# Kernel optimization log

Hardware: AMD Instinct MI355X
Metric: run time of the kernel (lower is better)

Reference implementation:

```python
import jax, jax.numpy as jnp
import numpy as np

N = 100000      # nodes
E = 1600000     # edges (avg degree 16)
IN = 128
HID = 128
OUT = 128
G = 512         # graphs in batch


def setup_inputs() -> dict:
    key = jax.random.key(0)
    ks = jax.random.split(key, 8)
    x = jax.random.normal(ks[0], (N, IN), dtype=jnp.float32)
    edge_index = jax.random.randint(ks[1], (2, E), 0, N, dtype=jnp.int64)
    batch = jnp.sort(jax.random.randint(ks[2], (N,), 0, G, dtype=jnp.int64))
    # GCNConv params: weight (glorot-ish) + zero bias, per layer
    W1 = jax.random.normal(ks[3], (IN, HID), dtype=jnp.float32) / np.sqrt(IN)
    b1 = jnp.zeros((HID,), jnp.float32)
    W2 = jax.random.normal(ks[4], (HID, OUT), dtype=jnp.float32) / np.sqrt(HID)
    b2 = jnp.zeros((OUT,), jnp.float32)
    return {"x": x, "edge_index": edge_index, "batch": batch,
            "W1": W1, "b1": b1, "W2": W2, "b2": b2}


def _gcn_layer(h, W, b, src, dst, norm, n):
    # linear transform then normalized scatter-add aggregation
    h = h @ W                                  # [N, F_out]
    msg = h[src] * norm[:, None]               # [E+N, F_out]
    out = jax.ops.segment_sum(msg, dst, num_segments=n)
    return out + b


def reference(x, edge_index, batch, W1, b1, W2, b2):
    x = x.astype(jnp.float32)
    n = x.shape[0]
    # GCNConv adds self-loops and uses symmetric deg^-1/2 normalization
    loop = jnp.arange(n)
    src = jnp.concatenate([edge_index[0], loop])
    dst = jnp.concatenate([edge_index[1], loop])
    deg = jax.ops.segment_sum(jnp.ones_like(dst, dtype=x.dtype), dst, num_segments=n)
    dis = jnp.where(deg > 0, jax.lax.rsqrt(jnp.maximum(deg, 1.0)), 0.0)
    norm = dis[src] * dis[dst]                 # [E+N]

    h = jax.nn.relu(_gcn_layer(x, W1, b1, src, dst, norm, n))
    # dropout p=0.0 -> identity
    h = jax.nn.relu(_gcn_layer(h, W2, b2, src, dst, norm, n))

    # global_mean_pool over batch ids
    sums = jax.ops.segment_sum(h, batch, num_segments=G)          # [G, OUT]
    counts = jax.ops.segment_sum(jnp.ones((n,), h.dtype), batch, num_segments=G)
    return sums / jnp.maximum(counts, 1.0)[:, None]
```

## Files before the change

### kernel.cpp

```cpp
#include <hip/hip_runtime.h>
#include <stddef.h>


#define F 128
#define EB 4096
#define BSH 9

typedef unsigned int uint;
typedef unsigned short ushort;
typedef __attribute__((ext_vector_type(8))) short s16x8;
typedef __attribute__((ext_vector_type(4))) float f32x4;

__device__ __forceinline__ float bf_lo(uint v) { return __uint_as_float(v << 16); }
__device__ __forceinline__ float bf_hi(uint v) { return __uint_as_float(v & 0xffff0000u); }
__device__ __forceinline__ ushort f2bf(float f) {
    uint u = __float_as_uint(f);
    u += 0x7fffu + ((u >> 16) & 1u);
    return (ushort)(u >> 16);
}
__device__ __forceinline__ uint pack_bf2(float lo, float hi) {
    return (uint)f2bf(lo) | ((uint)f2bf(hi) << 16);
}

__device__ __forceinline__ int scan256_incl(int* s, int t, int v) {
    s[t] = v;
    __syncthreads();
#pragma unroll
    for (int d = 1; d < 256; d <<= 1) {
        int y = (t >= d) ? s[t - d] : 0;
        __syncthreads();
        s[t] += y;
        __syncthreads();
    }
    return s[t];
}


__global__ __launch_bounds__(256) void passA_kernel(const int* __restrict__ ei,
                                                    int* __restrict__ bucket_cnt,
                                                    int e, int nbuc) {
    __shared__ int h[256];
    int t = threadIdx.x;
    h[t] = 0;
    __syncthreads();
    for (int i = blockIdx.x * 256 + t; i < e; i += gridDim.x * 256)
        atomicAdd(&h[ei[e + i] >> BSH], 1);
    __syncthreads();
    if (t < nbuc && h[t]) atomicAdd(&bucket_cnt[t], h[t]);
}


__global__ __launch_bounds__(256) void scanb_kernel(const int* __restrict__ bucket_cnt,
                                                    int* __restrict__ bucket_base,
                                                    int* __restrict__ gcur, int nbuc) {
    __shared__ int aux[256];
    int t = threadIdx.x;
    int v = (t < nbuc) ? bucket_cnt[t] : 0;
    int incl = scan256_incl(aux, t, v);
    int base = incl - v;
    bucket_base[t] = base;
    gcur[t] = base;
    if (t == nbuc - 1) bucket_base[nbuc] = incl;
}


__global__ __launch_bounds__(256) void passB_kernel(const int* __restrict__ ei,
                                                    int* __restrict__ gcur,
                                                    uint2* __restrict__ ebuf, int e) {
    __shared__ uint2 stage[EB];
    __shared__ int h[256], start[256], cur[256], claim[256], aux[256];
    int t = threadIdx.x;
    h[t] = 0;
    __syncthreads();
    int base = blockIdx.x * EB;
    int s_r[16], d_r[16];
#pragma unroll
    for (int k = 0; k < 16; ++k) {
        int i = base + k * 256 + t;
        int sv = -1, dv = 0;
        if (i < e) {
            sv = ei[i];
            dv = ei[e + i];
            atomicAdd(&h[dv >> BSH], 1);
        }
        s_r[k] = sv; d_r[k] = dv;
    }
    __syncthreads();
    int hv = h[t];
    int incl = scan256_incl(aux, t, hv);
    start[t] = incl - hv;
    cur[t]   = incl - hv;
    claim[t] = (hv > 0) ? atomicAdd(&gcur[t], hv) : 0;
    __syncthreads();
#pragma unroll
    for (int k = 0; k < 16; ++k) {
        if (s_r[k] >= 0) {
            int b = d_r[k] >> BSH;
            int r = atomicAdd(&cur[b], 1);
            stage[r] = make_uint2((uint)s_r[k], (uint)d_r[k]);
        }
    }
    __syncthreads();
    int valid = min(EB, e - base);
#pragma unroll
    for (int k = 0; k < 16; ++k) {
        int idx = k * 256 + t;
        if (idx < valid) {
            uint2 ed = stage[idx];
            int b = (int)(ed.y >> BSH);
            ebuf[claim[b] + (idx - start[b])] = ed;
        }
    }
}


__global__ __launch_bounds__(256) void passC1_kernel(const uint2* __restrict__ ebuf,
                                                     const int* __restrict__ bucket_base,
                                                     int* __restrict__ rp,
                                                     float* __restrict__ dis, int n) {
    __shared__ int h[512];
    __shared__ int aux[256];
    int t = threadIdx.x, b = blockIdx.x;
    int v0 = b << BSH;
    h[t] = 0; h[t + 256] = 0;
    __syncthreads();
    int ebeg = bucket_base[b], eend = bucket_base[b + 1];
    for (int i = ebeg + t; i < eend; i += 256)
        atomicAdd(&h[(int)ebuf[i].y - v0], 1);
    __syncthreads();
#pragma unroll
    for (int k = 0; k < 2; ++k) {
        int v = v0 + t + k * 256;
        if (v < n) dis[v] = rsqrtf((float)(h[t + k * 256] + 1));
    }
    int p = h[2 * t] + h[2 * t + 1];
    int incl = scan256_incl(aux, t, p);
    int ex = incl - p;
    int v = v0 + 2 * t;
    if (v <= n)     rp[v]     = ebeg + ex;
    if (v + 1 <= n) rp[v + 1] = ebeg + ex + h[2 * t];
}


__global__ __launch_bounds__(256) void passC2_kernel(const uint2* __restrict__ ebuf,
                                                     const int* __restrict__ bucket_base,
                                                     const int* __restrict__ rp,
                                                     const float* __restrict__ dis,
                                                     uint2* __restrict__ ew, int n) {
    __shared__ int cur[512];
    __shared__ float dl[512];
    int t = threadIdx.x, b = blockIdx.x;
    int v0 = b << BSH;
#pragma unroll
    for (int k = 0; k < 2; ++k) {
        int idx = t + k * 256, v = v0 + idx;
        cur[idx] = (v < n) ? rp[v] : 0;
        dl[idx]  = (v < n) ? dis[v] : 0.f;
    }
    __syncthreads();
    int ebeg = bucket_base[b], eend = bucket_base[b + 1];
    for (int i = ebeg + t; i < eend; i += 256) {
        uint2 ed = ebuf[i];
        int s = (int)ed.x, d = (int)ed.y - v0;
        float w = dis[s] * dl[d];
        int p = atomicAdd(&cur[d], 1);
        ew[p] = make_uint2(ed.x, __float_as_uint(w));
    }
}


__global__ void wprep_kernel(const float* __restrict__ W1, const float* __restrict__ W2,
                             ushort* __restrict__ wt) {
    int idx = blockIdx.x * 256 + threadIdx.x;
    if (idx >= 2 * F * F) return;
    int m = idx >> 14;
    int c = (idx >> 7) & 127;
    int r = idx & 127;
    const float* W = m ? W2 : W1;
    float w = W[r * F + c];
    ushort hi = f2bf(w);
    float whi = __uint_as_float((uint)hi << 16);
    ushort lo = f2bf(w - whi);
    wt[((m * 2 + 0) * F + c) * F + r] = hi;
    wt[((m * 2 + 1) * F + c) * F + r] = lo;
}


template <bool F32IN>
__global__ __launch_bounds__(256) void gemm_mfma_kernel(const float* __restrict__ Af,
                                                        const uint* __restrict__ Ab,
                                                        const ushort* __restrict__ wt,
                                                        ushort* __restrict__ C, int n) {
    __shared__ uint4 As4[2048];
    const int t = threadIdx.x;
    const int w = t >> 6;
    const int lane = t & 63;
    const int r0 = blockIdx.x * 128;

#pragma unroll
    for (int p = 0; p < 8; ++p) {
        int g = p * 256 + t;
        int row = g >> 4;
        int c8 = g & 15;
        uint4 v = make_uint4(0u, 0u, 0u, 0u);
        if (r0 + row < n) {
            if (F32IN) {
                const float* a = Af + (size_t)(r0 + row) * F + c8 * 8;
                float4 f0 = *(const float4*)a;
                float4 f1 = *(const float4*)(a + 4);
                v.x = pack_bf2(f0.x, f0.y);
                v.y = pack_bf2(f0.z, f0.w);
                v.z = pack_bf2(f1.x, f1.y);
                v.w = pack_bf2(f1.z, f1.w);
            } else {
                v = *(const uint4*)(Ab + ((size_t)(r0 + row) * F + c8 * 8) / 2);
            }
        }
        As4[row * 16 + (c8 ^ (row & 7))] = v;
    }
    __syncthreads();

    const s16x8* As8 = (const s16x8*)As4;
    const uint4* Bh = (const uint4*)wt;
    const uint4* Bl = Bh + F * 16;

    f32x4 acc[2][8];
#pragma unroll
    for (int i = 0; i < 2; ++i)
#pragma unroll
        for (int c = 0; c < 8; ++c) acc[i][c] = (f32x4){0.f, 0.f, 0.f, 0.f};

    const int kg = lane >> 4;
    const int lr = lane & 15;

#pragma unroll
    for (int ks = 0; ks < 4; ++ks) {
        s16x8 a0, a1;
        {
            int row = w * 32 + lr;
            a0 = As8[row * 16 + ((ks * 4 + kg) ^ (row & 7))];
            row += 16;
            a1 = As8[row * 16 + ((ks * 4 + kg) ^ (row & 7))];
        }
#pragma unroll
        for (int c = 0; c < 8; ++c) {
            int col = c * 16 + lr;
            int gidx = col * 16 + ks * 4 + kg;
            uint4 bhu = Bh[gidx];
            uint4 blu = Bl[gidx];
            s16x8 bh = *(const s16x8*)&bhu;
            s16x8 bl = *(const s16x8*)&blu;
            acc[0][c] = __builtin_amdgcn_mfma_f32_16x16x32_bf16(a0, bh, acc[0][c], 0, 0, 0);
            acc[0][c] = __builtin_amdgcn_mfma_f32_16x16x32_bf16(a0, bl, acc[0][c], 0, 0, 0);
            acc[1][c] = __builtin_amdgcn_mfma_f32_16x16x32_bf16(a1, bh, acc[1][c], 0, 0, 0);
            acc[1][c] = __builtin_amdgcn_mfma_f32_16x16x32_bf16(a1, bl, acc[1][c], 0, 0, 0);
        }
    }

    __syncthreads();
    ushort* Cs = (ushort*)As4;
#pragma unroll
    for (int i = 0; i < 2; ++i)
#pragma unroll
        for (int c = 0; c < 8; ++c)
#pragma unroll
            for (int reg = 0; reg < 4; ++reg) {
                int row = w * 32 + i * 16 + (lane >> 4) * 4 + reg;
                int col = c * 16 + lr;
                Cs[row * F + col] = f2bf(acc[i][c][reg]);
            }
    __syncthreads();
#pragma unroll
    for (int p = 0; p < 8; ++p) {
        int g = p * 256 + t;
        int row = g >> 4;
        int c8 = g & 15;
        if (r0 + row < n)
            *(uint4*)(C + (size_t)(r0 + row) * F + c8 * 8) = As4[g];
    }
}


__global__ __launch_bounds__(256) void agg_kernel(const uint* __restrict__ h2,
                                                  const int* __restrict__ rp,
                                                  const uint2* __restrict__ ew,
                                                  const float* __restrict__ dis,
                                                  const float* __restrict__ bias,
                                                  uint* __restrict__ out2, int n) {
    int wid = __builtin_amdgcn_readfirstlane(threadIdx.x >> 6);
    int node = blockIdx.x * 4 + wid;
    if (node >= n) return;
    int lane = threadIdx.x & 63;
    float di = dis[node];
    int beg = rp[node], end = rp[node + 1];
    uint hv = h2[((uint)node << 6) | lane];
    float w0 = di * di;
    float ax = w0 * bf_lo(hv);
    float ay = w0 * bf_hi(hv);
    int j = beg;
    for (; j + 8 <= end; j += 8) {
        uint2 E0 = ew[j],     E1 = ew[j + 1], E2 = ew[j + 2], E3 = ew[j + 3];
        uint2 E4 = ew[j + 4], E5 = ew[j + 5], E6 = ew[j + 6], E7 = ew[j + 7];
        uint v0 = h2[(E0.x << 6) | lane];
        uint v1 = h2[(E1.x << 6) | lane];
        uint v2 = h2[(E2.x << 6) | lane];
        uint v3 = h2[(E3.x << 6) | lane];
        uint v4 = h2[(E4.x << 6) | lane];
        uint v5 = h2[(E5.x << 6) | lane];
        uint v6 = h2[(E6.x << 6) | lane];
        uint v7 = h2[(E7.x << 6) | lane];
        float w0e = __uint_as_float(E0.y), w1e = __uint_as_float(E1.y);
        float w2e = __uint_as_float(E2.y), w3e = __uint_as_float(E3.y);
        float w4e = __uint_as_float(E4.y), w5e = __uint_as_float(E5.y);
        float w6e = __uint_as_float(E6.y), w7e = __uint_as_float(E7.y);
        ax = fmaf(w0e, bf_lo(v0), ax); ay = fmaf(w0e, bf_hi(v0), ay);
        ax = fmaf(w1e, bf_lo(v1), ax); ay = fmaf(w1e, bf_hi(v1), ay);
        ax = fmaf(w2e, bf_lo(v2), ax); ay = fmaf(w2e, bf_hi(v2), ay);
        ax = fmaf(w3e, bf_lo(v3), ax); ay = fmaf(w3e, bf_hi(v3), ay);
        ax = fmaf(w4e, bf_lo(v4), ax); ay = fmaf(w4e, bf_hi(v4), ay);
        ax = fmaf(w5e, bf_lo(v5), ax); ay = fmaf(w5e, bf_hi(v5), ay);
        ax = fmaf(w6e, bf_lo(v6), ax); ay = fmaf(w6e, bf_hi(v6), ay);
        ax = fmaf(w7e, bf_lo(v7), ax); ay = fmaf(w7e, bf_hi(v7), ay);
    }
    for (; j < end; ++j) {
        uint2 E0 = ew[j];
        uint v0 = h2[(E0.x << 6) | lane];
        float w0e = __uint_as_float(E0.y);
        ax = fmaf(w0e, bf_lo(v0), ax);
        ay = fmaf(w0e, bf_hi(v0), ay);
    }
    float2 b = ((const float2*)bias)[lane];
    ax = fmaxf(ax + b.x, 0.f);
    ay = fmaxf(ay + b.y, 0.f);
    out2[((uint)node << 6) | lane] = pack_bf2(ax, ay);
}


__global__ __launch_bounds__(256) void pool_kernel(const uint* __restrict__ h2,
                                                   const int* __restrict__ batch,
                                                   float* __restrict__ out, int n) {
    __shared__ int sb[2];
    __shared__ float red[4][F];
    int g = blockIdx.x;
    int t = threadIdx.x;
    if (t < 2) {
        int target = g + t;
        int lo = 0, hi = n;
        while (lo < hi) {
            int mid = (lo + hi) >> 1;
            if (batch[mid] < target) lo = mid + 1; else hi = mid;
        }
        sb[t] = lo;
    }
    __syncthreads();
    int start = sb[0], end = sb[1];
    int lane = t & 63, w = t >> 6;
    float sx = 0.f, sy = 0.f;
    for (int i = start + w; i < end; i += 4) {
        uint v = h2[((uint)i << 6) | lane];
        sx += bf_lo(v);
        sy += bf_hi(v);
    }
    red[w][lane * 2] = sx;
    red[w][lane * 2 + 1] = sy;
    __syncthreads();
    if (w == 0) {
        float s0 = red[0][lane * 2] + red[1][lane * 2] + red[2][lane * 2] + red[3][lane * 2];
        float s1 = red[0][lane * 2 + 1] + red[1][lane * 2 + 1] + red[2][lane * 2 + 1] + red[3][lane * 2 + 1];
        float inv = 1.f / fmaxf((float)(end - start), 1.f);
        out[(size_t)g * F + lane * 2]     = s0 * inv;
        out[(size_t)g * F + lane * 2 + 1] = s1 * inv;
    }
}


extern "C" void kernel_launch(void* const* d_in, const int* in_sizes, int n_in,
                              void* d_out, int out_size, void* d_ws, size_t ws_size,
                              hipStream_t stream) {
    const float* x     = (const float*)d_in[0];
    const int*   ei    = (const int*)d_in[1];
    const int*   batch = (const int*)d_in[2];
    const float* W1    = (const float*)d_in[3];
    const float* b1    = (const float*)d_in[4];
    const float* W2    = (const float*)d_in[5];
    const float* b2    = (const float*)d_in[6];
    float* out = (float*)d_out;

    const int n = in_sizes[0] / F;
    const int e = in_sizes[1] / 2;
    const int g = out_size / F;
    const int nbuc = (n + (1 << BSH) - 1) >> BSH;

    char* ws = (char*)d_ws;
    size_t off = 0;
    auto alloc = [&](size_t bytes) -> char* {
        char* p = ws + off;
        off += (bytes + 255) & ~(size_t)255;
        return p;
    };
    float*  dis   = (float*)alloc((size_t)n * 4);
    int*    rp    = (int*)  alloc((size_t)(n + 1) * 4);
    int*    bcnt  = (int*)  alloc(256 * 4);
    int*    bbase = (int*)  alloc(257 * 4);
    int*    gcur  = (int*)  alloc(256 * 4);
    uint2*  ebuf  = (uint2*)alloc((size_t)e * 8);
    uint2*  ew    = (uint2*)alloc((size_t)e * 8);
    ushort* wt    = (ushort*)alloc((size_t)4 * F * F * 2);
    uint*   hbuf  = (uint*) alloc((size_t)n * F * 2);
    uint*   abuf  = (uint*) alloc((size_t)n * F * 2);
    (void)ws_size;

    hipMemsetAsync(bcnt, 0, 256 * 4, stream);
    wprep_kernel<<<(2 * F * F + 255) / 256, 256, 0, stream>>>(W1, W2, wt);
    passA_kernel<<<256, 256, 0, stream>>>(ei, bcnt, e, nbuc);
    scanb_kernel<<<1, 256, 0, stream>>>(bcnt, bbase, gcur, nbuc);
    passB_kernel<<<(e + EB - 1) / EB, 256, 0, stream>>>(ei, gcur, ebuf, e);
    passC1_kernel<<<nbuc, 256, 0, stream>>>(ebuf, bbase, rp, dis, n);
    passC2_kernel<<<nbuc, 256, 0, stream>>>(ebuf, bbase, rp, dis, ew, n);

    const int gblk = (n + 127) / 128;
    gemm_mfma_kernel<true><<<gblk, 256, 0, stream>>>(x, nullptr, wt, (ushort*)hbuf, n);
    agg_kernel<<<(n + 3) / 4, 256, 0, stream>>>(hbuf, rp, ew, dis, b1, abuf, n);
    gemm_mfma_kernel<false><<<gblk, 256, 0, stream>>>(nullptr, abuf, wt + 2 * F * F, (ushort*)hbuf, n);
    agg_kernel<<<(n + 3) / 4, 256, 0, stream>>>(hbuf, rp, ew, dis, b2, abuf, n);
    pool_kernel<<<g, 256, 0, stream>>>(abuf, batch, out, n);
}
```

Measured before the change: 381.4 us.

## Persistent register-resident-B GEMM, split-edge aggregation, fuse weight prep with scan

The GEMM becomes a persistent kernel over 128-row strips. Each wave keeps its 32-column slice of the hi/lo bf16 weights in registers, and the next strip is prefetched into registers while the current one runs MFMAs from a double-buffered LDS tile. The aggregation kernel now gives each node two waves that take alternating edges and combine partials through shared memory, adding parallelism per node at the cost of a block barrier and more blocks. The weight-prep kernel and the bucket scan are merged into one launch to save a kernel launch.

```diff
diff --git a/kernel.cpp b/kernel.cpp
--- a/kernel.cpp
+++ b/kernel.cpp
@@ -50,129 +50,24 @@
 }
 
 
-__global__ __launch_bounds__(256) void scanb_kernel(const int* __restrict__ bucket_cnt,
-                                                    int* __restrict__ bucket_base,
-                                                    int* __restrict__ gcur, int nbuc) {
-    __shared__ int aux[256];
-    int t = threadIdx.x;
-    int v = (t < nbuc) ? bucket_cnt[t] : 0;
-    int incl = scan256_incl(aux, t, v);
-    int base = incl - v;
-    bucket_base[t] = base;
-    gcur[t] = base;
-    if (t == nbuc - 1) bucket_base[nbuc] = incl;
-}
-
-
-__global__ __launch_bounds__(256) void passB_kernel(const int* __restrict__ ei,
-                                                    int* __restrict__ gcur,
-                                                    uint2* __restrict__ ebuf, int e) {
-    __shared__ uint2 stage[EB];
-    __shared__ int h[256], start[256], cur[256], claim[256], aux[256];
-    int t = threadIdx.x;
-    h[t] = 0;
-    __syncthreads();
-    int base = blockIdx.x * EB;
-    int s_r[16], d_r[16];
-#pragma unroll
-    for (int k = 0; k < 16; ++k) {
-        int i = base + k * 256 + t;
-        int sv = -1, dv = 0;
-        if (i < e) {
-            sv = ei[i];
-            dv = ei[e + i];
-            atomicAdd(&h[dv >> BSH], 1);
-        }
-        s_r[k] = sv; d_r[k] = dv;
-    }
-    __syncthreads();
-    int hv = h[t];
-    int incl = scan256_incl(aux, t, hv);
-    start[t] = incl - hv;
-    cur[t]   = incl - hv;
-    claim[t] = (hv > 0) ? atomicAdd(&gcur[t], hv) : 0;
-    __syncthreads();
-#pragma unroll
-    for (int k = 0; k < 16; ++k) {
-        if (s_r[k] >= 0) {
-            int b = d_r[k] >> BSH;
-            int r = atomicAdd(&cur[b], 1);
-            stage[r] = make_uint2((uint)s_r[k], (uint)d_r[k]);
-        }
-    }
-    __syncthreads();
-    int valid = min(EB, e - base);
-#pragma unroll
-    for (int k = 0; k < 16; ++k) {
-        int idx = k * 256 + t;
-        if (idx < valid) {
-            uint2 ed = stage[idx];
-            int b = (int)(ed.y >> BSH);
-            ebuf[claim[b] + (idx - start[b])] = ed;
-        }
-    }
-}
-
-
-__global__ __launch_bounds__(256) void passC1_kernel(const uint2* __restrict__ ebuf,
-                                                     const int* __restrict__ bucket_base,
-                                                     int* __restrict__ rp,
-                                                     float* __restrict__ dis, int n) {
-    __shared__ int h[512];
-    __shared__ int aux[256];
-    int t = threadIdx.x, b = blockIdx.x;
-    int v0 = b << BSH;
-    h[t] = 0; h[t + 256] = 0;
-    __syncthreads();
-    int ebeg = bucket_base[b], eend = bucket_base[b + 1];
-    for (int i = ebeg + t; i < eend; i += 256)
-        atomicAdd(&h[(int)ebuf[i].y - v0], 1);
-    __syncthreads();
-#pragma unroll
-    for (int k = 0; k < 2; ++k) {
-        int v = v0 + t + k * 256;
-        if (v < n) dis[v] = rsqrtf((float)(h[t + k * 256] + 1));
-    }
-    int p = h[2 * t] + h[2 * t + 1];
-    int incl = scan256_incl(aux, t, p);
-    int ex = incl - p;
-    int v = v0 + 2 * t;
-    if (v <= n)     rp[v]     = ebeg + ex;
-    if (v + 1 <= n) rp[v + 1] = ebeg + ex + h[2 * t];
-}
-
-
-__global__ __launch_bounds__(256) void passC2_kernel(const uint2* __restrict__ ebuf,
-                                                     const int* __restrict__ bucket_base,
-                                                     const int* __restrict__ rp,
-                                                     const float* __restrict__ dis,
-                                                     uint2* __restrict__ ew, int n) {
-    __shared__ int cur[512];
-    __shared__ float dl[512];
-    int t = threadIdx.x, b = blockIdx.x;
-    int v0 = b << BSH;
-#pragma unroll
-    for (int k = 0; k < 2; ++k) {
-        int idx = t + k * 256, v = v0 + idx;
-        cur[idx] = (v < n) ? rp[v] : 0;
-        dl[idx]  = (v < n) ? dis[v] : 0.f;
-    }
-    __syncthreads();
-    int ebeg = bucket_base[b], eend = bucket_base[b + 1];
-    for (int i = ebeg + t; i < eend; i += 256) {
-        uint2 ed = ebuf[i];
-        int s = (int)ed.x, d = (int)ed.y - v0;
-        float w = dis[s] * dl[d];
-        int p = atomicAdd(&cur[d], 1);
-        ew[p] = make_uint2(ed.x, __float_as_uint(w));
-    }
-}
-
-
-__global__ void wprep_kernel(const float* __restrict__ W1, const float* __restrict__ W2,
-                             ushort* __restrict__ wt) {
+__global__ __launch_bounds__(256) void prep_scan_kernel(const float* __restrict__ W1,
+                                                        const float* __restrict__ W2,
+                                                        ushort* __restrict__ wt,
+                                                        const int* __restrict__ bucket_cnt,
+                                                        int* __restrict__ bucket_base,
+                                                        int* __restrict__ gcur, int nbuc) {
+    if (blockIdx.x == 128) {
+        __shared__ int aux[256];
+        int t = threadIdx.x;
+        int v = (t < nbuc) ? bucket_cnt[t] : 0;
+        int incl = scan256_incl(aux, t, v);
+        int base = incl - v;
+        bucket_base[t] = base;
+        gcur[t] = base;
+        if (t == nbuc - 1) bucket_base[nbuc] = incl;
+        return;
+    }
     int idx = blockIdx.x * 256 + threadIdx.x;
-    if (idx >= 2 * F * F) return;
     int m = idx >> 14;
     int c = (idx >> 7) & 127;
     int r = idx & 127;
@@ -186,97 +81,221 @@
 }
 
 
+__global__ __launch_bounds__(256) void passB_kernel(const int* __restrict__ ei,
+                                                    int* __restrict__ gcur,
+                                                    uint2* __restrict__ ebuf, int e) {
+    __shared__ uint2 stage[EB];
+    __shared__ int h[256], start[256], cur[256], claim[256], aux[256];
+    int t = threadIdx.x;
+    h[t] = 0;
+    __syncthreads();
+    int base = blockIdx.x * EB;
+    int s_r[16], d_r[16];
+#pragma unroll
+    for (int k = 0; k < 16; ++k) {
+        int i = base + k * 256 + t;
+        int sv = -1, dv = 0;
+        if (i < e) {
+            sv = ei[i];
+            dv = ei[e + i];
+            atomicAdd(&h[dv >> BSH], 1);
+        }
+        s_r[k] = sv; d_r[k] = dv;
+    }
+    __syncthreads();
+    int hv = h[t];
+    int incl = scan256_incl(aux, t, hv);
+    start[t] = incl - hv;
+    cur[t]   = incl - hv;
+    claim[t] = (hv > 0) ? atomicAdd(&gcur[t], hv) : 0;
+    __syncthreads();
+#pragma unroll
+    for (int k = 0; k < 16; ++k) {
+        if (s_r[k] >= 0) {
+            int b = d_r[k] >> BSH;
+            int r = atomicAdd(&cur[b], 1);
+            stage[r] = make_uint2((uint)s_r[k], (uint)d_r[k]);
+        }
+    }
+    __syncthreads();
+    int valid = min(EB, e - base);
+#pragma unroll
+    for (int k = 0; k < 16; ++k) {
+        int idx = k * 256 + t;
+        if (idx < valid) {
+            uint2 ed = stage[idx];
+            int b = (int)(ed.y >> BSH);
+            ebuf[claim[b] + (idx - start[b])] = ed;
+        }
+    }
+}
+
+
+__global__ __launch_bounds__(256) void passC1_kernel(const uint2* __restrict__ ebuf,
+                                                     const int* __restrict__ bucket_base,
+                                                     int* __restrict__ rp,
+                                                     float* __restrict__ dis, int n) {
+    __shared__ int h[512];
+    __shared__ int aux[256];
+    int t = threadIdx.x, b = blockIdx.x;
+    int v0 = b << BSH;
+    h[t] = 0; h[t + 256] = 0;
+    __syncthreads();
+    int ebeg = bucket_base[b], eend = bucket_base[b + 1];
+    for (int i = ebeg + t; i < eend; i += 256)
+        atomicAdd(&h[(int)ebuf[i].y - v0], 1);
+    __syncthreads();
+#pragma unroll
+    for (int k = 0; k < 2; ++k) {
+        int v = v0 + t + k * 256;
+        if (v < n) dis[v] = rsqrtf((float)(h[t + k * 256] + 1));
+    }
+    int p = h[2 * t] + h[2 * t + 1];
+    int incl = scan256_incl(aux, t, p);
+    int ex = incl - p;
+    int v = v0 + 2 * t;
+    if (v <= n)     rp[v]     = ebeg + ex;
+    if (v + 1 <= n) rp[v + 1] = ebeg + ex + h[2 * t];
+}
+
+
+__global__ __launch_bounds__(256) void passC2_kernel(const uint2* __restrict__ ebuf,
+                                                     const int* __restrict__ bucket_base,
+                                                     const int* __restrict__ rp,
+                                                     const float* __restrict__ dis,
+                                                     uint2* __restrict__ ew, int n) {
+    __shared__ int cur[512];
+    __shared__ float dl[512];
+    int t = threadIdx.x, b = blockIdx.x;
+    int v0 = b << BSH;
+#pragma unroll
+    for (int k = 0; k < 2; ++k) {
+        int idx = t + k * 256, v = v0 + idx;
+        cur[idx] = (v < n) ? rp[v] : 0;
+        dl[idx]  = (v < n) ? dis[v] : 0.f;
+    }
+    __syncthreads();
+    int ebeg = bucket_base[b], eend = bucket_base[b + 1];
+    for (int i = ebeg + t; i < eend; i += 256) {
+        uint2 ed = ebuf[i];
+        int s = (int)ed.x, d = (int)ed.y - v0;
+        float w = dis[s] * dl[d];
+        int p = atomicAdd(&cur[d], 1);
+        ew[p] = make_uint2(ed.x, __float_as_uint(w));
+    }
+}
+
+
 template <bool F32IN>
 __global__ __launch_bounds__(256) void gemm_mfma_kernel(const float* __restrict__ Af,
                                                         const uint* __restrict__ Ab,
                                                         const ushort* __restrict__ wt,
-                                                        ushort* __restrict__ C, int n) {
-    __shared__ uint4 As4[2048];
+                                                        ushort* __restrict__ C,
+                                                        int n, int nstrips) {
+    __shared__ uint4 As4[2][2048];
     const int t = threadIdx.x;
     const int w = t >> 6;
     const int lane = t & 63;
-    const int r0 = blockIdx.x * 128;
-
-#pragma unroll
-    for (int p = 0; p < 8; ++p) {
-        int g = p * 256 + t;
-        int row = g >> 4;
-        int c8 = g & 15;
-        uint4 v = make_uint4(0u, 0u, 0u, 0u);
-        if (r0 + row < n) {
-            if (F32IN) {
-                const float* a = Af + (size_t)(r0 + row) * F + c8 * 8;
-                float4 f0 = *(const float4*)a;
-                float4 f1 = *(const float4*)(a + 4);
-                v.x = pack_bf2(f0.x, f0.y);
-                v.y = pack_bf2(f0.z, f0.w);
-                v.z = pack_bf2(f1.x, f1.y);
-                v.w = pack_bf2(f1.z, f1.w);
-            } else {
-                v = *(const uint4*)(Ab + ((size_t)(r0 + row) * F + c8 * 8) / 2);
-            }
-        }
-        As4[row * 16 + (c8 ^ (row & 7))] = v;
-    }
-    __syncthreads();
-
-    const s16x8* As8 = (const s16x8*)As4;
-    const uint4* Bh = (const uint4*)wt;
-    const uint4* Bl = Bh + F * 16;
-
-    f32x4 acc[2][8];
-#pragma unroll
-    for (int i = 0; i < 2; ++i)
-#pragma unroll
-        for (int c = 0; c < 8; ++c) acc[i][c] = (f32x4){0.f, 0.f, 0.f, 0.f};
-
     const int kg = lane >> 4;
     const int lr = lane & 15;
 
-#pragma unroll
-    for (int ks = 0; ks < 4; ++ks) {
-        s16x8 a0, a1;
-        {
-            int row = w * 32 + lr;
-            a0 = As8[row * 16 + ((ks * 4 + kg) ^ (row & 7))];
-            row += 16;
-            a1 = As8[row * 16 + ((ks * 4 + kg) ^ (row & 7))];
-        }
-#pragma unroll
-        for (int c = 0; c < 8; ++c) {
-            int col = c * 16 + lr;
-            int gidx = col * 16 + ks * 4 + kg;
-            uint4 bhu = Bh[gidx];
-            uint4 blu = Bl[gidx];
-            s16x8 bh = *(const s16x8*)&bhu;
-            s16x8 bl = *(const s16x8*)&blu;
-            acc[0][c] = __builtin_amdgcn_mfma_f32_16x16x32_bf16(a0, bh, acc[0][c], 0, 0, 0);
-            acc[0][c] = __builtin_amdgcn_mfma_f32_16x16x32_bf16(a0, bl, acc[0][c], 0, 0, 0);
-            acc[1][c] = __builtin_amdgcn_mfma_f32_16x16x32_bf16(a1, bh, acc[1][c], 0, 0, 0);
-            acc[1][c] = __builtin_amdgcn_mfma_f32_16x16x32_bf16(a1, bl, acc[1][c], 0, 0, 0);
-        }
-    }
-
-    __syncthreads();
-    ushort* Cs = (ushort*)As4;
-#pragma unroll
-    for (int i = 0; i < 2; ++i)
-#pragma unroll
-        for (int c = 0; c < 8; ++c)
-#pragma unroll
-            for (int reg = 0; reg < 4; ++reg) {
-                int row = w * 32 + i * 16 + (lane >> 4) * 4 + reg;
-                int col = c * 16 + lr;
-                Cs[row * F + col] = f2bf(acc[i][c][reg]);
+    const uint4* Bg = (const uint4*)wt;
+    s16x8 bfr[2][2][4];
+#pragma unroll
+    for (int part = 0; part < 2; ++part)
+#pragma unroll
+        for (int c = 0; c < 2; ++c)
+#pragma unroll
+            for (int ks = 0; ks < 4; ++ks) {
+                int col = w * 32 + c * 16 + lr;
+                uint4 bu = Bg[part * F * 16 + col * 16 + ks * 4 + kg];
+                bfr[part][c][ks] = *(const s16x8*)&bu;
             }
-    __syncthreads();
-#pragma unroll
-    for (int p = 0; p < 8; ++p) {
-        int g = p * 256 + t;
-        int row = g >> 4;
-        int c8 = g & 15;
-        if (r0 + row < n)
-            *(uint4*)(C + (size_t)(r0 + row) * F + c8 * 8) = As4[g];
+
+    auto load_strip = [&](int strip, uint4* st) {
+        int r0 = strip * 128;
+#pragma unroll
+        for (int p = 0; p < 8; ++p) {
+            int g = p * 256 + t;
+            int row = g >> 4, q = g & 15;
+            int c8 = q ^ (row & 7);
+            uint4 v = make_uint4(0u, 0u, 0u, 0u);
+            int gr = r0 + row;
+            if (gr < n) {
+                if (F32IN) {
+                    const float* a = Af + (size_t)gr * F + c8 * 8;
+                    float4 f0 = *(const float4*)a;
+                    float4 f1 = *(const float4*)(a + 4);
+                    v.x = pack_bf2(f0.x, f0.y);
+                    v.y = pack_bf2(f0.z, f0.w);
+                    v.z = pack_bf2(f1.x, f1.y);
+                    v.w = pack_bf2(f1.z, f1.w);
+                } else {
+                    v = *(const uint4*)(Ab + (size_t)gr * 64 + c8 * 4);
+                }
+            }
+            st[p] = v;
+        }
+    };
+
+    int s = blockIdx.x;
+    if (s >= nstrips) return;
+    uint4 st[8];
+    load_strip(s, st);
+    int buf = 0;
+    for (; s < nstrips; s += gridDim.x) {
+#pragma unroll
+        for (int p = 0; p < 8; ++p) As4[buf][p * 256 + t] = st[p];
+        __syncthreads();
+        int s2 = s + gridDim.x;
+        if (s2 < nstrips) load_strip(s2, st);
+
+        f32x4 acc[8][2];
+#pragma unroll
+        for (int r = 0; r < 8; ++r)
+#pragma unroll
+            for (int c = 0; c < 2; ++c) acc[r][c] = (f32x4){0.f, 0.f, 0.f, 0.f};
+
+        const s16x8* As8 = (const s16x8*)As4[buf];
+#pragma unroll
+        for (int ks = 0; ks < 4; ++ks) {
+            s16x8 afr[8];
+#pragma unroll
+            for (int r = 0; r < 8; ++r) {
+                int row = r * 16 + lr;
+                afr[r] = As8[row * 16 + ((ks * 4 + kg) ^ (row & 7))];
+            }
+#pragma unroll
+            for (int r = 0; r < 8; ++r)
+#pragma unroll
+                for (int c = 0; c < 2; ++c) {
+                    acc[r][c] = __builtin_amdgcn_mfma_f32_16x16x32_bf16(afr[r], bfr[0][c][ks], acc[r][c], 0, 0, 0);
+                    acc[r][c] = __builtin_amdgcn_mfma_f32_16x16x32_bf16(afr[r], bfr[1][c][ks], acc[r][c], 0, 0, 0);
+                }
+        }
+        __syncthreads();
+
+        ushort* Cs = (ushort*)As4[buf];
+#pragma unroll
+        for (int r = 0; r < 8; ++r)
+#pragma unroll
+            for (int c = 0; c < 2; ++c)
+#pragma unroll
+                for (int reg = 0; reg < 4; ++reg) {
+                    int row = r * 16 + kg * 4 + reg;
+                    int col = w * 32 + c * 16 + lr;
+                    Cs[row * F + col] = f2bf(acc[r][c][reg]);
+                }
+        __syncthreads();
+        int r0 = s * 128;
+#pragma unroll
+        for (int p = 0; p < 8; ++p) {
+            int g = p * 256 + t;
+            int row = g >> 4, c8 = g & 15;
+            if (r0 + row < n)
+                *(uint4*)(C + (size_t)(r0 + row) * F + c8 * 8) = As4[buf][g];
+        }
+        buf ^= 1;
     }
 }
 
@@ -287,52 +306,51 @@
                                                   const float* __restrict__ dis,
                                                   const float* __restrict__ bias,
                                                   uint* __restrict__ out2, int n) {
-    int wid = __builtin_amdgcn_readfirstlane(threadIdx.x >> 6);
-    int node = blockIdx.x * 4 + wid;
-    if (node >= n) return;
-    int lane = threadIdx.x & 63;
-    float di = dis[node];
-    int beg = rp[node], end = rp[node + 1];
-    uint hv = h2[((uint)node << 6) | lane];
-    float w0 = di * di;
-    float ax = w0 * bf_lo(hv);
-    float ay = w0 * bf_hi(hv);
-    int j = beg;
-    for (; j + 8 <= end; j += 8) {
-        uint2 E0 = ew[j],     E1 = ew[j + 1], E2 = ew[j + 2], E3 = ew[j + 3];
-        uint2 E4 = ew[j + 4], E5 = ew[j + 5], E6 = ew[j + 6], E7 = ew[j + 7];
+    __shared__ float redx[2][64], redy[2][64];
+    int t = threadIdx.x;
+    int w = t >> 6;
+    int lane = t & 63;
+    int pair = w >> 1;
+    int sub = w & 1;
+    int node = blockIdx.x * 2 + pair;
+    bool active = node < n;
+    float ax = 0.f, ay = 0.f;
+    int beg = 0, end = 0;
+    if (active) { beg = rp[node]; end = rp[node + 1]; }
+    int j = beg + sub;
+    for (; j + 6 < end; j += 8) {
+        uint2 E0 = ew[j], E1 = ew[j + 2], E2 = ew[j + 4], E3 = ew[j + 6];
         uint v0 = h2[(E0.x << 6) | lane];
         uint v1 = h2[(E1.x << 6) | lane];
         uint v2 = h2[(E2.x << 6) | lane];
         uint v3 = h2[(E3.x << 6) | lane];
-        uint v4 = h2[(E4.x << 6) | lane];
-        uint v5 = h2[(E5.x << 6) | lane];
-        uint v6 = h2[(E6.x << 6) | lane];
-        uint v7 = h2[(E7.x << 6) | lane];
         float w0e = __uint_as_float(E0.y), w1e = __uint_as_float(E1.y);
         float w2e = __uint_as_float(E2.y), w3e = __uint_as_float(E3.y);
-        float w4e = __uint_as_float(E4.y), w5e = __uint_as_float(E5.y);
-        float w6e = __uint_as_float(E6.y), w7e = __uint_as_float(E7.y);
         ax = fmaf(w0e, bf_lo(v0), ax); ay = fmaf(w0e, bf_hi(v0), ay);
         ax = fmaf(w1e, bf_lo(v1), ax); ay = fmaf(w1e, bf_hi(v1), ay);
         ax = fmaf(w2e, bf_lo(v2), ax); ay = fmaf(w2e, bf_hi(v2), ay);
         ax = fmaf(w3e, bf_lo(v3), ax); ay = fmaf(w3e, bf_hi(v3), ay);
-        ax = fmaf(w4e, bf_lo(v4), ax); ay = fmaf(w4e, bf_hi(v4), ay);
-        ax = fmaf(w5e, bf_lo(v5), ax); ay = fmaf(w5e, bf_hi(v5), ay);
-        ax = fmaf(w6e, bf_lo(v6), ax); ay = fmaf(w6e, bf_hi(v6), ay);
-        ax = fmaf(w7e, bf_lo(v7), ax); ay = fmaf(w7e, bf_hi(v7), ay);
-    }
-    for (; j < end; ++j) {
+    }
+    for (; j < end; j += 2) {
         uint2 E0 = ew[j];
         uint v0 = h2[(E0.x << 6) | lane];
         float w0e = __uint_as_float(E0.y);
         ax = fmaf(w0e, bf_lo(v0), ax);
         ay = fmaf(w0e, bf_hi(v0), ay);
     }
-    float2 b = ((const float2*)bias)[lane];
-    ax = fmaxf(ax + b.x, 0.f);
-    ay = fmaxf(ay + b.y, 0.f);
-    out2[((uint)node << 6) | lane] = pack_bf2(ax, ay);
+    if (sub == 1) { redx[pair][lane] = ax; redy[pair][lane] = ay; }
+    __syncthreads();
+    if (active && sub == 0) {
+        float di = dis[node];
+        float w0 = di * di;
+        uint hv = h2[((uint)node << 6) | lane];
+        ax += redx[pair][lane] + w0 * bf_lo(hv);
+        ay += redy[pair][lane] + w0 * bf_hi(hv);
+        float2 b = ((const float2*)bias)[lane];
+        ax = fmaxf(ax + b.x, 0.f);
+        ay = fmaxf(ay + b.y, 0.f);
+        out2[((uint)node << 6) | lane] = pack_bf2(ax, ay);
+    }
 }
 
 
@@ -411,17 +429,17 @@
     (void)ws_size;
 
     hipMemsetAsync(bcnt, 0, 256 * 4, stream);
-    wprep_kernel<<<(2 * F * F + 255) / 256, 256, 0, stream>>>(W1, W2, wt);
     passA_kernel<<<256, 256, 0, stream>>>(ei, bcnt, e, nbuc);
-    scanb_kernel<<<1, 256, 0, stream>>>(bcnt, bbase, gcur, nbuc);
+    prep_scan_kernel<<<129, 256, 0, stream>>>(W1, W2, wt, bcnt, bbase, gcur, nbuc);
     passB_kernel<<<(e + EB - 1) / EB, 256, 0, stream>>>(ei, gcur, ebuf, e);
     passC1_kernel<<<nbuc, 256, 0, stream>>>(ebuf, bbase, rp, dis, n);
     passC2_kernel<<<nbuc, 256, 0, stream>>>(ebuf, bbase, rp, dis, ew, n);
 
-    const int gblk = (n + 127) / 128;
-    gemm_mfma_kernel<true><<<gblk, 256, 0, stream>>>(x, nullptr, wt, (ushort*)hbuf, n);
-    agg_kernel<<<(n + 3) / 4, 256, 0, stream>>>(hbuf, rp, ew, dis, b1, abuf, n);
-    gemm_mfma_kernel<false><<<gblk, 256, 0, stream>>>(nullptr, abuf, wt + 2 * F * F, (ushort*)hbuf, n);
-    agg_kernel<<<(n + 3) / 4, 256, 0, stream>>>(hbuf, rp, ew, dis, b2, abuf, n);
+    const int nstrips = (n + 127) / 128;
+    const int ggrid = nstrips < 261 ? nstrips : 261;
+    gemm_mfma_kernel<true><<<ggrid, 256, 0, stream>>>(x, nullptr, wt, (ushort*)hbuf, n, nstrips);
+    agg_kernel<<<(n + 1) / 2, 256, 0, stream>>>(hbuf, rp, ew, dis, b1, abuf, n);
+    gemm_mfma_kernel<false><<<ggrid, 256, 0, stream>>>(nullptr, abuf, wt + 2 * F * F, (ushort*)hbuf, n, nstrips);
+    agg_kernel<<<(n + 1) / 2, 256, 0, stream>>>(hbuf, rp, ew, dis, b2, abuf, n);
     pool_kernel<<<g, 256, 0, stream>>>(abuf, batch, out, n);
 }
```

After: 442.3 us. 16.0% more time.
